# Kernel tuning notes

Hardware: AMD Instinct MI355X
Metric: run time of the kernel (lower is better)

The kernel has to match this reference:

```python
import jax, jax.numpy as jnp
import numpy as np

D_IN = 784
D = 768          # hidden_dim
R = 8            # num_rels
L = 3            # num_layers
B = 64           # graphs in batch
N = 32768        # total nodes
E = 262144       # total edges


def _layer_norm(x, g, b, eps=1e-5):
    m = x.mean(-1, keepdims=True)
    v = x.var(-1, keepdims=True)
    return (x - m) / jnp.sqrt(v + eps) * g + b


def setup_inputs() -> dict:
    key = jax.random.key(0)
    ks = jax.random.split(key, 24)
    s = 0.02
    inp = {
        "type_vec": jax.random.normal(ks[0], (N, 16), jnp.float32),
        "code_vec": jax.random.normal(ks[1], (N, D), jnp.float32),
        # input_proj: Linear(784,768) + LayerNorm(768)
        "W_in": jax.random.normal(ks[2], (D_IN, D), jnp.float32) * s,
        "b_in": jnp.zeros((D,), jnp.float32),
        "ln_in_g": jnp.ones((D,), jnp.float32),
        "ln_in_b": jnp.zeros((D,), jnp.float32),
        # RGCN layers (basis regularizer, num_bases=num_rels -> per-relation W)
        "W_rel": jax.random.normal(ks[3], (L, R, D, D), jnp.float32) * s,
        "W_loop": jax.random.normal(ks[4], (L, D, D), jnp.float32) * s,
        "rgcn_bias": jnp.zeros((L, D), jnp.float32),
        "ln_g": jnp.ones((L, D), jnp.float32),
        "ln_b": jnp.zeros((L, D), jnp.float32),
        # global attention pooling gate MLP: 768 -> 384 -> 1
        "Wg1": jax.random.normal(ks[5], (D, D // 2), jnp.float32) * s,
        "bg1": jnp.zeros((D // 2,), jnp.float32),
        "Wg2": jax.random.normal(ks[6], (D // 2, 1), jnp.float32) * s,
        "bg2": jnp.zeros((1,), jnp.float32),
        # classifier: 768 -> 512 (+LN) -> 2
        "Wc1": jax.random.normal(ks[7], (D, 512), jnp.float32) * s,
        "bc1": jnp.zeros((512,), jnp.float32),
        "ln_c_g": jnp.ones((512,), jnp.float32),
        "ln_c_b": jnp.zeros((512,), jnp.float32),
        "Wc2": jax.random.normal(ks[8], (512, 2), jnp.float32) * s,
        "bc2": jnp.zeros((2,), jnp.float32),
        # graph structure
        "src": jax.random.randint(ks[9], (E,), 0, N, jnp.int64),
        "dst": jax.random.randint(ks[10], (E,), 0, N, jnp.int64),
        "edge_type": jax.random.randint(ks[11], (E,), 0, R, jnp.int64),
        "node_graph": jnp.sort(jax.random.randint(ks[12], (N,), 0, B, jnp.int64)),
        "num_graphs": B,
    }
    return inp


def reference(type_vec, code_vec, W_in, b_in, ln_in_g, ln_in_b,
              W_rel, W_loop, rgcn_bias, ln_g, ln_b,
              Wg1, bg1, Wg2, bg2, Wc1, bc1, ln_c_g, ln_c_b, Wc2, bc2,
              src, dst, edge_type, node_graph, num_graphs):
    # input projection
    h = jnp.concatenate([type_vec, code_vec], axis=-1)           # [N, 784]
    h = jax.nn.gelu(_layer_norm(h @ W_in + b_in, ln_in_g, ln_in_b), approximate=False)
    n_nodes = h.shape[0]
    n_layers, n_rels = W_rel.shape[0], W_rel.shape[1]

    for l in range(n_layers):
        agg = jnp.zeros_like(h)
        for r in range(n_rels):
            # relation-specific transform, then gather->mask->scatter-add
            msg = (h @ W_rel[l, r])[src] * (edge_type == r).astype(h.dtype)[:, None]  # [E, D]
            agg = agg + jax.ops.segment_sum(msg, dst, num_segments=n_nodes)
        h_new = agg + rgcn_bias[l] + h @ W_loop[l]               # DGL: agg + bias + self-loop
        h = jax.nn.gelu(_layer_norm(h_new, ln_g[l], ln_b[l]), approximate=False)

    # global attention pooling (segment softmax over nodes of each graph)
    gate = (jax.nn.gelu(h @ Wg1 + bg1, approximate=False) @ Wg2 + bg2)[:, 0]  # [N]
    gmax = jax.ops.segment_max(gate, node_graph, num_segments=num_graphs)
    e = jnp.exp(gate - gmax[node_graph])
    denom = jax.ops.segment_sum(e, node_graph, num_segments=num_graphs)
    w = e / denom[node_graph]
    graph_repr = jax.ops.segment_sum(w[:, None] * h, node_graph, num_segments=num_graphs)  # [B, D]

    # classifier head
    z = jax.nn.gelu(_layer_norm(graph_repr @ Wc1 + bc1, ln_c_g, ln_c_b), approximate=False)
    logits = z @ Wc2 + bc2
    return jax.nn.log_softmax(logits, axis=-1)
```

## Files before the change

### kernel.cpp

```cpp
#include <hip/hip_runtime.h>
#include <hip/hip_bf16.h>

typedef __hip_bfloat16 bf16;
typedef __attribute__((ext_vector_type(8))) __bf16 bf16x8;
typedef __attribute__((ext_vector_type(4))) float f32x4;

#define N_NODES 32768
#define N_EDGES 262144
#define DIM 768
#define NGR 64
#define KIN 800
#define KSTACK 6912
#define NKEY (N_NODES * 8)

#define GLOBAL_AS __attribute__((address_space(1)))
#define LDS_AS __attribute__((address_space(3)))

__device__ __forceinline__ float gelu_f(float x) {
    return 0.5f * x * (1.0f + erff(x * 0.70710678118654752f));
}
__device__ __forceinline__ float bfu(unsigned short v) {
    union { unsigned u; float f; } x; x.u = (unsigned)v << 16; return x.f;
}
__device__ __forceinline__ unsigned short fbf(float f) {
    bf16 t = __float2bfloat16(f); return *(unsigned short*)&t;
}

__global__ __launch_bounds__(256)
void tcast_k(const float* __restrict__ in, bf16* __restrict__ out, int I, int O,
             int Ipad, int ostride) {
    __shared__ float t[32][33];
    const int i0 = blockIdx.x * 32, o0 = blockIdx.y * 32;
    const int tx = threadIdx.x & 31, ty = threadIdx.x >> 5;
#pragma unroll
    for (int q = 0; q < 4; ++q) {
        int i = i0 + ty + q * 8, o = o0 + tx;
        t[ty + q * 8][tx] = (i < I) ? in[(size_t)i * O + o] : 0.0f;
    }
    __syncthreads();
#pragma unroll
    for (int q = 0; q < 4; ++q) {
        int o = o0 + ty + q * 8, i = i0 + tx;
        if (i < Ipad) out[(size_t)o * ostride + i] = __float2bfloat16(t[tx][ty + q * 8]);
    }
}

__global__ __launch_bounds__(256)
void wprep_k(const float* __restrict__ W_rel, const float* __restrict__ W_loop,
             bf16* __restrict__ Wst) {
    __shared__ float t[32][33];
    const int z = blockIdx.z, l = z / 9, q = z % 9;
    const float* in = (q < 8) ? W_rel + ((size_t)(l * 8 + q)) * DIM * DIM
                              : W_loop + (size_t)l * DIM * DIM;
    bf16* out = Wst + (size_t)l * DIM * KSTACK + (q < 8 ? (q + 1) * DIM : 0);
    const int i0 = blockIdx.x * 32, o0 = blockIdx.y * 32;
    const int tx = threadIdx.x & 31, ty = threadIdx.x >> 5;
#pragma unroll
    for (int qq = 0; qq < 4; ++qq)
        t[ty + qq * 8][tx] = in[(size_t)(i0 + ty + qq * 8) * DIM + o0 + tx];
    __syncthreads();
#pragma unroll
    for (int qq = 0; qq < 4; ++qq)
        out[(size_t)(o0 + ty + qq * 8) * KSTACK + i0 + tx] =
            __float2bfloat16(t[tx][ty + qq * 8]);
}

__global__ __launch_bounds__(256)
void concat_k(const float* __restrict__ tv, const float* __restrict__ cv, bf16* __restrict__ X) {
    const int n = blockIdx.x;
    for (int c = threadIdx.x; c < KIN; c += 256) {
        float v = 0.0f;
        if (c < 16) v = tv[(size_t)n * 16 + c];
        else if (c < 784) v = cv[(size_t)n * DIM + (c - 16)];
        X[(size_t)n * KIN + c] = __float2bfloat16(v);
    }
}

__global__ __launch_bounds__(256)
void hist2_k(const int* __restrict__ dst, const int* __restrict__ et, int* __restrict__ deg) {
    int e = blockIdx.x * 256 + threadIdx.x;
    if (e < N_EDGES) atomicAdd(&deg[dst[e] * 8 + et[e]], 1);
}

__global__ __launch_bounds__(1024)
void scan2_k(const int* __restrict__ deg, int* __restrict__ rp, int* __restrict__ cur) {
    __shared__ int part[1024];
    const int t = threadIdx.x;
    const int base_i = t * 256;
    int s = 0;
    for (int i = 0; i < 256; ++i) s += deg[base_i + i];
    part[t] = s; __syncthreads();
    for (int st = 1; st < 1024; st <<= 1) {
        int v = (t >= st) ? part[t - st] : 0;
        __syncthreads();
        part[t] += v;
        __syncthreads();
    }
    int run = part[t] - s;
    for (int i = 0; i < 256; ++i) {
        int d = deg[base_i + i];
        rp[base_i + i] = run; cur[base_i + i] = run;
        run += d;
    }
    if (t == 1023) rp[NKEY] = run;
}

__global__ __launch_bounds__(256)
void place2_k(const int* __restrict__ src, const int* __restrict__ dst,
              const int* __restrict__ et, int* __restrict__ cur, int* __restrict__ eidx) {
    int e = blockIdx.x * 256 + threadIdx.x;
    if (e >= N_EDGES) return;
    int pos = atomicAdd(&cur[dst[e] * 8 + et[e]], 1);
    eidx[pos] = src[e];
}

template <int NC>
__global__ __launch_bounds__(256)
void gather2_k(const bf16* __restrict__ h, const int* __restrict__ rp2,
               const int* __restrict__ eidx, bf16* __restrict__ AGG, int rbase) {
    const int wave = threadIdx.x >> 6, lane = threadIdx.x & 63;
    const int n = blockIdx.x * 4 + wave;
    const int c0 = 2 * lane;
    unsigned short* outrow = (unsigned short*)&AGG[(size_t)n * (NC * DIM)];
    const int* bp = &rp2[n * 8 + rbase];
#pragma unroll 1
    for (int sel = 0; sel < NC; ++sel) {
        const int s = bp[sel], e = bp[sel + 1];
        float2 f[6] = {};
        for (int t = s; t < e; ++t) {
            const unsigned short* hs = (const unsigned short*)&h[(size_t)eidx[t] * DIM];
#pragma unroll
            for (int j = 0; j < 6; ++j) {
                ushort2 u = *(const ushort2*)&hs[c0 + j * 128];
                f[j].x += bfu(u.x); f[j].y += bfu(u.y);
            }
        }
#pragma unroll
        for (int j = 0; j < 6; ++j) {
            ushort2 o; o.x = fbf(f[j].x); o.y = fbf(f[j].y);
            *(ushort2*)&outrow[sel * DIM + c0 + j * 128] = o;
        }
    }
}

template <int ACCUM>
__global__ __launch_bounds__(512, 2)
void gemm256(const bf16* __restrict__ A1, int S1, int K1,
             const bf16* __restrict__ A2, int S2,
             const bf16* __restrict__ BT, int ldb,
             float* __restrict__ OUT, int Nn, int Ktot, int nbx) {
    __shared__ __align__(16) unsigned short lA[128 * 32];
    __shared__ __align__(16) unsigned short lB[256 * 32];
    const int nblk = gridDim.x;
    const int qx = nblk >> 3;
    const int bid = blockIdx.x;
    const int wgid = (bid & 7) * qx + (bid >> 3);
    const int bx = wgid % nbx, by = wgid / nbx;
    const int bn = bx * 256, bm = by * 128;
    const int tid = threadIdx.x;
    const int wave = tid >> 6, lane = tid & 63;
    const int wr = wave >> 2, wc = wave & 3;
    const int l15 = lane & 15, lg = lane >> 4;

    f32x4 acc[4][4] = {};

    for (int k0 = 0; k0 < Ktot; k0 += 32) {
        const bf16* Ab; int koff, stA;
        if (k0 < K1) { Ab = A1; koff = k0; stA = S1; }
        else         { Ab = A2; koff = k0 - K1; stA = S2; }
        {
            const int row = tid >> 2, k8 = tid & 3;
            const bf16* ga = Ab + (size_t)(bm + row) * stA + koff + k8 * 8;
            __builtin_amdgcn_global_load_lds((const GLOBAL_AS void*)ga,
                (LDS_AS void*)&lA[(wave * 64) * 8], 16, 0, 0);
        }
#pragma unroll
        for (int qq = 0; qq < 2; ++qq) {
            const int c = qq * 512 + tid;
            const int row = c >> 2, k8 = c & 3;
            const bf16* gb = BT + (size_t)(bn + row) * ldb + k0 + k8 * 8;
            __builtin_amdgcn_global_load_lds((const GLOBAL_AS void*)gb,
                (LDS_AS void*)&lB[((qq * 8 + wave) * 64) * 8], 16, 0, 0);
        }
        __syncthreads();
        bf16x8 af[4], bfr[4];
#pragma unroll
        for (int mi = 0; mi < 4; ++mi)
            af[mi] = *reinterpret_cast<const bf16x8*>(&lA[(wr * 64 + mi * 16 + l15) * 32 + lg * 8]);
#pragma unroll
        for (int ni = 0; ni < 4; ++ni)
            bfr[ni] = *reinterpret_cast<const bf16x8*>(&lB[(wc * 64 + ni * 16 + l15) * 32 + lg * 8]);
#pragma unroll
        for (int mi = 0; mi < 4; ++mi)
#pragma unroll
            for (int ni = 0; ni < 4; ++ni)
                acc[mi][ni] = __builtin_amdgcn_mfma_f32_16x16x32_bf16(af[mi], bfr[ni], acc[mi][ni], 0, 0, 0);
        __syncthreads();
    }

#pragma unroll
    for (int mi = 0; mi < 4; ++mi)
#pragma unroll
        for (int ni = 0; ni < 4; ++ni) {
            const int r0 = bm + wr * 64 + mi * 16 + lg * 4;
            const int c0 = bn + wc * 64 + ni * 16 + l15;
#pragma unroll
            for (int i = 0; i < 4; ++i) {
                size_t idx = (size_t)(r0 + i) * Nn + c0;
                float v = acc[mi][ni][i];
                if (ACCUM) v += OUT[idx];
                OUT[idx] = v;
            }
        }
}

template <int ACCUM>
__global__ __launch_bounds__(256, 2)
void gemm_bt(const bf16* __restrict__ A1, int S1, int K1,
             const bf16* __restrict__ A2, int S2,
             const bf16* __restrict__ BT, int ldb,
             float* __restrict__ OUT, int Nn, int Ktot) {
    __shared__ __align__(16) unsigned short lA[128 * 32];
    __shared__ __align__(16) unsigned short lB[128 * 32];
    const int bn = blockIdx.x * 128;
    const int bm = blockIdx.y * 128;
    const int tid = threadIdx.x;
    const int wave = tid >> 6, lane = tid & 63;
    const int wr = wave >> 1, wc = wave & 1;
    const int l15 = lane & 15, lg = lane >> 4;

    f32x4 acc[4][4] = {};

    for (int k0 = 0; k0 < Ktot; k0 += 32) {
        const bf16* Ab; int koff, stA;
        if (k0 < K1) { Ab = A1; koff = k0; stA = S1; }
        else         { Ab = A2; koff = k0 - K1; stA = S2; }
#pragma unroll
        for (int q = 0; q < 2; ++q) {
            int c = wave * 128 + q * 64 + lane;
            int row = c >> 2, k8 = c & 3;
            const bf16* ga = Ab + (size_t)(bm + row) * stA + koff + k8 * 8;
            const bf16* gb = BT + (size_t)(bn + row) * ldb + k0 + k8 * 8;
            __builtin_amdgcn_global_load_lds((const GLOBAL_AS void*)ga,
                (LDS_AS void*)&lA[(wave * 128 + q * 64) * 8], 16, 0, 0);
            __builtin_amdgcn_global_load_lds((const GLOBAL_AS void*)gb,
                (LDS_AS void*)&lB[(wave * 128 + q * 64) * 8], 16, 0, 0);
        }
        __syncthreads();
        bf16x8 af[4], bfr[4];
#pragma unroll
        for (int mi = 0; mi < 4; ++mi)
            af[mi] = *reinterpret_cast<const bf16x8*>(&lA[(wr * 64 + mi * 16 + l15) * 32 + lg * 8]);
#pragma unroll
        for (int ni = 0; ni < 4; ++ni)
            bfr[ni] = *reinterpret_cast<const bf16x8*>(&lB[(wc * 64 + ni * 16 + l15) * 32 + lg * 8]);
#pragma unroll
        for (int mi = 0; mi < 4; ++mi)
#pragma unroll
            for (int ni = 0; ni < 4; ++ni)
                acc[mi][ni] = __builtin_amdgcn_mfma_f32_16x16x32_bf16(af[mi], bfr[ni], acc[mi][ni], 0, 0, 0);
        __syncthreads();
    }

#pragma unroll
    for (int mi = 0; mi < 4; ++mi)
#pragma unroll
        for (int ni = 0; ni < 4; ++ni) {
            const int r0 = bm + wr * 64 + mi * 16 + lg * 4;
            const int c0 = bn + wc * 64 + ni * 16 + l15;
#pragma unroll
            for (int i = 0; i < 4; ++i) {
                size_t idx = (size_t)(r0 + i) * Nn + c0;
                float v = acc[mi][ni][i];
                if (ACCUM) v += OUT[idx];
                OUT[idx] = v;
            }
        }
}

__global__ __launch_bounds__(256)
void ln_gelu_k(const float* __restrict__ ACC, const float* __restrict__ bias,
               const float* __restrict__ g, const float* __restrict__ b,
               bf16* __restrict__ hout) {
    const int wave = threadIdx.x >> 6, lane = threadIdx.x & 63;
    const int n = blockIdx.x * 4 + wave;
    float x[12];
    float s = 0.f, ss = 0.f;
#pragma unroll
    for (int j = 0; j < 12; ++j) {
        int c = lane + j * 64;
        x[j] = ACC[(size_t)n * DIM + c] + bias[c];
        s += x[j]; ss += x[j] * x[j];
    }
#pragma unroll
    for (int m = 1; m < 64; m <<= 1) { s += __shfl_xor(s, m, 64); ss += __shfl_xor(ss, m, 64); }
    const float mean = s * (1.f / DIM);
    const float var = ss * (1.f / DIM) - mean * mean;
    const float rstd = rsqrtf(var + 1e-5f);
#pragma unroll
    for (int j = 0; j < 12; ++j) {
        int c = lane + j * 64;
        float y = (x[j] - mean) * rstd * g[c] + b[c];
        hout[(size_t)n * DIM + c] = __float2bfloat16(gelu_f(y));
    }
}

__global__ __launch_bounds__(256)
void gate_k(const float* __restrict__ G1, const float* __restrict__ bg1,
            const float* __restrict__ Wg2, const float* __restrict__ bg2,
            float* __restrict__ gate) {
    const int wave = threadIdx.x >> 6, lane = threadIdx.x & 63;
    const int n = blockIdx.x * 4 + wave;
    float acc = 0.f;
#pragma unroll
    for (int j = 0; j < 6; ++j) {
        int c = lane + j * 64;
        float xv = G1[(size_t)n * 384 + c] + bg1[c];
        acc += gelu_f(xv) * Wg2[c];
    }
#pragma unroll
    for (int m = 1; m < 64; m <<= 1) acc += __shfl_xor(acc, m, 64);
    if (lane == 0) gate[n] = acc + bg2[0];
}

__device__ __forceinline__ int lower_bound_ng(const int* ng, int key) {
    int lo = 0, hi = N_NODES;
    while (lo < hi) { int mid = (lo + hi) >> 1; if (ng[mid] < key) lo = mid + 1; else hi = mid; }
    return lo;
}

__global__ __launch_bounds__(256)
void seg_stats_k(const float* __restrict__ gate, const int* __restrict__ ng,
                 float* __restrict__ gmax, float* __restrict__ gden) {
    __shared__ float red[256];
    const int b = blockIdx.x, t = threadIdx.x;
    const int start = lower_bound_ng(ng, b), end = lower_bound_ng(ng, b + 1);
    float m = -1e30f;
    for (int n = start + t; n < end; n += 256) m = fmaxf(m, gate[n]);
    red[t] = m; __syncthreads();
    for (int s = 128; s > 0; s >>= 1) { if (t < s) red[t] = fmaxf(red[t], red[t + s]); __syncthreads(); }
    const float gm = red[0]; __syncthreads();
    float ssum = 0.f;
    for (int n = start + t; n < end; n += 256) ssum += expf(gate[n] - gm);
    red[t] = ssum; __syncthreads();
    for (int s = 128; s > 0; s >>= 1) { if (t < s) red[t] += red[t + s]; __syncthreads(); }
    if (t == 0) { gmax[b] = gm; gden[b] = fmaxf(red[0], 1e-30f); }
}

__global__ __launch_bounds__(768)
void pool_k(const bf16* __restrict__ h, const float* __restrict__ gate,
            const int* __restrict__ ng, const float* __restrict__ gmax,
            const float* __restrict__ gden, float* __restrict__ grep) {
    const int b = blockIdx.x, c = threadIdx.x;
    const int start = lower_bound_ng(ng, b), end = lower_bound_ng(ng, b + 1);
    const float gm = gmax[b], inv = 1.0f / gden[b];
    const unsigned short* hv = (const unsigned short*)h;
    float a0 = 0.f, a1 = 0.f;
    int n = start;
    for (; n + 1 < end; n += 2) {
        float w0 = expf(gate[n] - gm) * inv;
        float w1 = expf(gate[n + 1] - gm) * inv;
        a0 += w0 * bfu(hv[(size_t)n * DIM + c]);
        a1 += w1 * bfu(hv[(size_t)(n + 1) * DIM + c]);
    }
    if (n < end) a0 += expf(gate[n] - gm) * inv * bfu(hv[(size_t)n * DIM + c]);
    grep[(size_t)b * DIM + c] = a0 + a1;
}

__global__ __launch_bounds__(512)
void cls_k(const float* __restrict__ grep, const float* __restrict__ Wc1,
           const float* __restrict__ bc1, const float* __restrict__ lng,
           const float* __restrict__ lnb, const float* __restrict__ Wc2,
           const float* __restrict__ bc2, float* __restrict__ out) {
    __shared__ float gr[DIM];
    __shared__ float red[512];
    const int b = blockIdx.x, j = threadIdx.x;
    for (int c = j; c < DIM; c += 512) gr[c] = grep[(size_t)b * DIM + c];
    __syncthreads();
    float a = bc1[j];
#pragma unroll 4
    for (int k = 0; k < DIM; ++k) a = fmaf(gr[k], Wc1[(size_t)k * 512 + j], a);
    red[j] = a; __syncthreads();
    for (int s = 256; s > 0; s >>= 1) { if (j < s) red[j] += red[j + s]; __syncthreads(); }
    const float mean = red[0] * (1.f / 512.f);
    __syncthreads();
    red[j] = (a - mean) * (a - mean); __syncthreads();
    for (int s = 256; s > 0; s >>= 1) { if (j < s) red[j] += red[j + s]; __syncthreads(); }
    const float rstd = rsqrtf(red[0] * (1.f / 512.f) + 1e-5f);
    __syncthreads();
    const float z = gelu_f((a - mean) * rstd * lng[j] + lnb[j]);
    red[j] = z * Wc2[2 * j + 0]; __syncthreads();
    for (int s = 256; s > 0; s >>= 1) { if (j < s) red[j] += red[j + s]; __syncthreads(); }
    const float l0 = red[0] + bc2[0];
    __syncthreads();
    red[j] = z * Wc2[2 * j + 1]; __syncthreads();
    for (int s = 256; s > 0; s >>= 1) { if (j < s) red[j] += red[j + s]; __syncthreads(); }
    if (j == 0) {
        const float l1 = red[0] + bc2[1];
        const float mx = fmaxf(l0, l1);
        const float lse = mx + logf(expf(l0 - mx) + expf(l1 - mx));
        out[2 * b + 0] = l0 - lse;
        out[2 * b + 1] = l1 - lse;
    }
}

extern "C" void kernel_launch(void* const* d_in, const int* in_sizes, int n_in,
                              void* d_out, int out_size, void* d_ws, size_t ws_size,
                              hipStream_t stream) {
    const float* type_vec = (const float*)d_in[0];
    const float* code_vec = (const float*)d_in[1];
    const float* W_in     = (const float*)d_in[2];
    const float* b_in     = (const float*)d_in[3];
    const float* ln_in_g  = (const float*)d_in[4];
    const float* ln_in_b  = (const float*)d_in[5];
    const float* W_rel    = (const float*)d_in[6];
    const float* W_loop   = (const float*)d_in[7];
    const float* rgcn_bias= (const float*)d_in[8];
    const float* ln_g     = (const float*)d_in[9];
    const float* ln_b     = (const float*)d_in[10];
    const float* Wg1      = (const float*)d_in[11];
    const float* bg1      = (const float*)d_in[12];
    const float* Wg2      = (const float*)d_in[13];
    const float* bg2      = (const float*)d_in[14];
    const float* Wc1      = (const float*)d_in[15];
    const float* bc1      = (const float*)d_in[16];
    const float* ln_c_g   = (const float*)d_in[17];
    const float* ln_c_b   = (const float*)d_in[18];
    const float* Wc2      = (const float*)d_in[19];
    const float* bc2      = (const float*)d_in[20];
    const int* src        = (const int*)d_in[21];
    const int* dst        = (const int*)d_in[22];
    const int* etype      = (const int*)d_in[23];
    const int* node_graph = (const int*)d_in[24];

    char* ws = (char*)d_ws;

    auto need = [](int nc) -> size_t {
        size_t base = 0;
        auto al = [&](size_t sz) { base = (base + sz + 255) & ~(size_t)255; };
        al((size_t)N_NODES * DIM * 2);
        al((size_t)N_NODES * DIM * 4);
        al((size_t)DIM * KIN * 2);
        al((size_t)3 * DIM * KSTACK * 2);
        al((size_t)384 * DIM * 2);
        size_t open = base;
        al((size_t)N_NODES * nc * DIM * 2);
        al((size_t)(NKEY + 1) * 4);
        al((size_t)NKEY * 4);
        al((size_t)NKEY * 4);
        al((size_t)N_EDGES * 4);
        al((size_t)N_NODES * 4);
        al(256); al(256);
        al((size_t)NGR * DIM * 4);
        size_t xend = open + (size_t)N_NODES * KIN * 2;
        return base > xend ? base : xend;
    };
    int nc = 1;
    if (ws_size >= need(4)) nc = 4;
    else if (ws_size >= need(2)) nc = 2;

    size_t off = 0;
    auto alloc = [&](size_t sz) { size_t r = off; off = (off + sz + 255) & ~(size_t)255; return r; };
    bf16*  h_bf  = (bf16*)(ws + alloc((size_t)N_NODES * DIM * 2));
    float* ACC   = (float*)(ws + alloc((size_t)N_NODES * DIM * 4));
    bf16*  WinT  = (bf16*)(ws + alloc((size_t)DIM * KIN * 2));
    bf16*  Wst   = (bf16*)(ws + alloc((size_t)3 * DIM * KSTACK * 2));
    bf16*  Wg1T  = (bf16*)(ws + alloc((size_t)384 * DIM * 2));
    size_t open  = off;
    bf16*  AGG   = (bf16*)(ws + alloc((size_t)N_NODES * nc * DIM * 2));
    int*   rp2   = (int*)(ws + alloc((size_t)(NKEY + 1) * 4));
    int*   cur2  = (int*)(ws + alloc((size_t)NKEY * 4));
    int*   deg2  = (int*)(ws + alloc((size_t)NKEY * 4));
    int*   eidx  = (int*)(ws + alloc((size_t)N_EDGES * 4));
    float* gate  = (float*)(ws + alloc((size_t)N_NODES * 4));
    float* gmax  = (float*)(ws + alloc(256));
    float* gden  = (float*)(ws + alloc(256));
    float* grep  = (float*)(ws + alloc((size_t)NGR * DIM * 4));
    bf16*  Xbf   = (bf16*)(ws + open);
    float* G1    = ACC;

    tcast_k<<<dim3(25, 24), 256, 0, stream>>>(W_in, WinT, 784, DIM, KIN, KIN);
    wprep_k<<<dim3(24, 24, 27), 256, 0, stream>>>(W_rel, W_loop, Wst);
    tcast_k<<<dim3(24, 12), 256, 0, stream>>>(Wg1, Wg1T, DIM, 384, DIM, DIM);

    concat_k<<<N_NODES, 256, 0, stream>>>(type_vec, code_vec, Xbf);
    gemm256<0><<<768, 512, 0, stream>>>(Xbf, KIN, KIN, Xbf, KIN, WinT, KIN, ACC, DIM, KIN, 3);
    ln_gelu_k<<<N_NODES / 4, 256, 0, stream>>>(ACC, b_in, ln_in_g, ln_in_b, h_bf);

    hipMemsetAsync(deg2, 0, (size_t)NKEY * 4, stream);
    hist2_k<<<N_EDGES / 256, 256, 0, stream>>>(dst, etype, deg2);
    scan2_k<<<1, 1024, 0, stream>>>(deg2, rp2, cur2);
    place2_k<<<N_EDGES / 256, 256, 0, stream>>>(src, dst, etype, cur2, eidx);

    const int nchunks = 8 / nc;
    for (int l = 0; l < 3; ++l) {
        bf16* Wl = Wst + (size_t)l * DIM * KSTACK;
        for (int c = 0; c < nchunks; ++c) {
            const int rbase = c * nc;
            if (nc == 1)      gather2_k<1><<<N_NODES / 4, 256, 0, stream>>>(h_bf, rp2, eidx, AGG, rbase);
            else if (nc == 2) gather2_k<2><<<N_NODES / 4, 256, 0, stream>>>(h_bf, rp2, eidx, AGG, rbase);
            else              gather2_k<4><<<N_NODES / 4, 256, 0, stream>>>(h_bf, rp2, eidx, AGG, rbase);
            if (c == 0) {
                gemm256<0><<<768, 512, 0, stream>>>(
                    h_bf, DIM, DIM, AGG, nc * DIM, Wl, KSTACK, ACC, DIM, DIM + nc * DIM, 3);
            } else {
                gemm256<1><<<768, 512, 0, stream>>>(
                    AGG, nc * DIM, nc * DIM, AGG, nc * DIM,
                    Wl + (size_t)DIM * (1 + rbase), KSTACK, ACC, DIM, nc * DIM, 3);
            }
        }
        ln_gelu_k<<<N_NODES / 4, 256, 0, stream>>>(ACC, rgcn_bias + l * DIM, ln_g + l * DIM,
                                                   ln_b + l * DIM, h_bf);
    }

    gemm_bt<0><<<dim3(3, 256), 256, 0, stream>>>(
        h_bf, DIM, DIM, h_bf, DIM, Wg1T, DIM, G1, 384, DIM);
    gate_k<<<N_NODES / 4, 256, 0, stream>>>(G1, bg1, Wg2, bg2, gate);
    seg_stats_k<<<NGR, 256, 0, stream>>>(gate, node_graph, gmax, gden);
    pool_k<<<NGR, 768, 0, stream>>>(h_bf, gate, node_graph, gmax, gden, grep);

    cls_k<<<NGR, 512, 0, stream>>>(grep, Wc1, bc1, ln_c_g, ln_c_b, Wc2, bc2, (float*)d_out);
}
```

Before: 2.774 ms.

## Load GEMM B fragments directly from global and swizzle A tile in LDS

The GEMM kernel stops staging the weight (B) tile through LDS. Each wave now reads its B fragments straight from global memory into registers, while only the A tile goes through LDS, using an XOR swizzle to avoid bank conflicts. Launch bounds rise to allow 4 blocks per CU since LDS use is halved. This trades LDS traffic for redundant global/L2 reads of B across the two wave rows and more exposed global-load latency inside the k-loop.

```diff
diff --git a/kernel.cpp b/kernel.cpp
--- a/kernel.cpp
+++ b/kernel.cpp
@@ -144,16 +144,13 @@
 }
 
 template <int ACCUM>
-__global__ __launch_bounds__(512, 2)
-void gemm256(const bf16* __restrict__ A1, int S1, int K1,
-             const bf16* __restrict__ A2, int S2,
-             const bf16* __restrict__ BT, int ldb,
-             float* __restrict__ OUT, int Nn, int Ktot, int nbx) {
+__global__ __launch_bounds__(512, 4)
+void gemm_bl2(const bf16* __restrict__ A1, int S1, int K1,
+              const bf16* __restrict__ A2, int S2,
+              const bf16* __restrict__ BT, int ldb,
+              float* __restrict__ OUT, int Nn, int Ktot, int nbx) {
     __shared__ __align__(16) unsigned short lA[128 * 32];
-    __shared__ __align__(16) unsigned short lB[256 * 32];
-    const int nblk = gridDim.x;
-    const int qx = nblk >> 3;
-    const int bid = blockIdx.x;
+    const int nblk = gridDim.x, qx = nblk >> 3, bid = blockIdx.x;
     const int wgid = (bid & 7) * qx + (bid >> 3);
     const int bx = wgid % nbx, by = wgid / nbx;
     const int bn = bx * 256, bm = by * 128;
@@ -162,39 +159,46 @@
     const int wr = wave >> 2, wc = wave & 3;
     const int l15 = lane & 15, lg = lane >> 4;
 
+    const bf16* bp0 = BT + (size_t)(bn + wc * 64 +  0 + l15) * ldb + lg * 8;
+    const bf16* bp1 = BT + (size_t)(bn + wc * 64 + 16 + l15) * ldb + lg * 8;
+    const bf16* bp2 = BT + (size_t)(bn + wc * 64 + 32 + l15) * ldb + lg * 8;
+    const bf16* bp3 = BT + (size_t)(bn + wc * 64 + 48 + l15) * ldb + lg * 8;
+
     f32x4 acc[4][4] = {};
-
-    for (int k0 = 0; k0 < Ktot; k0 += 32) {
-        const bf16* Ab; int koff, stA;
-        if (k0 < K1) { Ab = A1; koff = k0; stA = S1; }
-        else         { Ab = A2; koff = k0 - K1; stA = S2; }
+    const int nkt = Ktot >> 5;
+
+    for (int kt = 0; kt < nkt; ++kt) {
+        const int kbase = kt * 32;
+        bf16x8 bq0 = *(const bf16x8*)(bp0 + kbase);
+        bf16x8 bq1 = *(const bf16x8*)(bp1 + kbase);
+        bf16x8 bq2 = *(const bf16x8*)(bp2 + kbase);
+        bf16x8 bq3 = *(const bf16x8*)(bp3 + kbase);
         {
-            const int row = tid >> 2, k8 = tid & 3;
-            const bf16* ga = Ab + (size_t)(bm + row) * stA + koff + k8 * 8;
+            const bf16* Ab; int stA, koff;
+            if (kbase < K1) { Ab = A1; stA = S1; koff = kbase; }
+            else            { Ab = A2; stA = S2; koff = kbase - K1; }
+            const int r = tid >> 2, s = tid & 3;
+            const int sc = (s ^ ((r >> 1) & 3)) * 8;
+            const bf16* ga = Ab + (size_t)(bm + r) * stA + koff + sc;
             __builtin_amdgcn_global_load_lds((const GLOBAL_AS void*)ga,
-                (LDS_AS void*)&lA[(wave * 64) * 8], 16, 0, 0);
-        }
-#pragma unroll
-        for (int qq = 0; qq < 2; ++qq) {
-            const int c = qq * 512 + tid;
-            const int row = c >> 2, k8 = c & 3;
-            const bf16* gb = BT + (size_t)(bn + row) * ldb + k0 + k8 * 8;
-            __builtin_amdgcn_global_load_lds((const GLOBAL_AS void*)gb,
-                (LDS_AS void*)&lB[((qq * 8 + wave) * 64) * 8], 16, 0, 0);
+                (LDS_AS void*)&lA[tid * 8], 16, 0, 0);
         }
         __syncthreads();
-        bf16x8 af[4], bfr[4];
-#pragma unroll
-        for (int mi = 0; mi < 4; ++mi)
-            af[mi] = *reinterpret_cast<const bf16x8*>(&lA[(wr * 64 + mi * 16 + l15) * 32 + lg * 8]);
-#pragma unroll
-        for (int ni = 0; ni < 4; ++ni)
-            bfr[ni] = *reinterpret_cast<const bf16x8*>(&lB[(wc * 64 + ni * 16 + l15) * 32 + lg * 8]);
-#pragma unroll
-        for (int mi = 0; mi < 4; ++mi)
-#pragma unroll
-            for (int ni = 0; ni < 4; ++ni)
-                acc[mi][ni] = __builtin_amdgcn_mfma_f32_16x16x32_bf16(af[mi], bfr[ni], acc[mi][ni], 0, 0, 0);
+
+        bf16x8 af[4];
+#pragma unroll
+        for (int mi = 0; mi < 4; ++mi) {
+            const int r = wr * 64 + mi * 16 + l15;
+            const int p = (lg ^ ((l15 >> 1) & 3)) * 8;
+            af[mi] = *(const bf16x8*)&lA[r * 32 + p];
+        }
+#pragma unroll
+        for (int mi = 0; mi < 4; ++mi) {
+            acc[mi][0] = __builtin_amdgcn_mfma_f32_16x16x32_bf16(af[mi], bq0, acc[mi][0], 0, 0, 0);
+            acc[mi][1] = __builtin_amdgcn_mfma_f32_16x16x32_bf16(af[mi], bq1, acc[mi][1], 0, 0, 0);
+            acc[mi][2] = __builtin_amdgcn_mfma_f32_16x16x32_bf16(af[mi], bq2, acc[mi][2], 0, 0, 0);
+            acc[mi][3] = __builtin_amdgcn_mfma_f32_16x16x32_bf16(af[mi], bq3, acc[mi][3], 0, 0, 0);
+        }
         __syncthreads();
     }
 
@@ -484,7 +488,7 @@
     tcast_k<<<dim3(24, 12), 256, 0, stream>>>(Wg1, Wg1T, DIM, 384, DIM, DIM);
 
     concat_k<<<N_NODES, 256, 0, stream>>>(type_vec, code_vec, Xbf);
-    gemm256<0><<<768, 512, 0, stream>>>(Xbf, KIN, KIN, Xbf, KIN, WinT, KIN, ACC, DIM, KIN, 3);
+    gemm_bl2<0><<<768, 512, 0, stream>>>(Xbf, KIN, KIN, Xbf, KIN, WinT, KIN, ACC, DIM, KIN, 3);
     ln_gelu_k<<<N_NODES / 4, 256, 0, stream>>>(ACC, b_in, ln_in_g, ln_in_b, h_bf);
 
     hipMemsetAsync(deg2, 0, (size_t)NKEY * 4, stream);
@@ -501,10 +505,10 @@
             else if (nc == 2) gather2_k<2><<<N_NODES / 4, 256, 0, stream>>>(h_bf, rp2, eidx, AGG, rbase);
             else              gather2_k<4><<<N_NODES / 4, 256, 0, stream>>>(h_bf, rp2, eidx, AGG, rbase);
             if (c == 0) {
-                gemm256<0><<<768, 512, 0, stream>>>(
+                gemm_bl2<0><<<768, 512, 0, stream>>>(
                     h_bf, DIM, DIM, AGG, nc * DIM, Wl, KSTACK, ACC, DIM, DIM + nc * DIM, 3);
             } else {
-                gemm256<1><<<768, 512, 0, stream>>>(
+                gemm_bl2<1><<<768, 512, 0, stream>>>(
                     AGG, nc * DIM, nc * DIM, AGG, nc * DIM,
                     Wl + (size_t)DIM * (1 + rbase), KSTACK, ACC, DIM, nc * DIM, 3);
             }
```

Result: slower. 3.694 ms (+33.2%).
